# Kernel optimization log

Measured on AMD Instinct MI355X. Metric: run time of the kernel, lower is better.

## Reference

```python
import jax, jax.numpy as jnp
import numpy as np

B, T, D, H = 4, 4096, 2048, 128  # head_size = embedding_size // num_heads = 2048 // 16

def setup_inputs() -> dict:
    key = jax.random.key(0)
    kx, kq, kk, kv = jax.random.split(key, 4)
    x = jax.random.normal(kx, (B, T, D), dtype=jnp.float32)
    # Dense kernels with normal(0.01) init as in the module
    Wq = 0.01 * jax.random.normal(kq, (D, H), dtype=jnp.float32)
    Wk = 0.01 * jax.random.normal(kk, (D, H), dtype=jnp.float32)
    Wv = 0.01 * jax.random.normal(kv, (D, H), dtype=jnp.float32)
    return {"x": x, "Wq": Wq, "Wk": Wk, "Wv": Wv}

def reference(x, Wq, Wk, Wv):
    # Q/K/V projections: Dense(features=head_size, use_bias=False)
    Q = jnp.einsum('BTD,DH->BTH', x, Wq)
    K = jnp.einsum('BTD,DH->BTH', x, Wk)
    V = jnp.einsum('BTD,DH->BTH', x, Wv)
    scale = 1.0 / jnp.sqrt(jnp.asarray(K.shape[-1], dtype=x.dtype))
    scores = jnp.einsum('BTH,BSH->BTS', Q, K) * scale  # (B, T, T)
    weights = jax.nn.softmax(scores, axis=-1)
    # dropout rate 0.0 (deterministic) -> identity
    out = jnp.einsum('BTS,BSH->BTH', weights, V)  # (B, T, H)
    return out
```

## Files before the change

### kernel.cpp

```cpp
#include <hip/hip_runtime.h>
#include <hip/hip_bf16.h>
#include <math.h>

#define B_ 4
#define T_ 4096
#define D_ 2048
#define H_ 128
#define M_ (B_*T_)

typedef __bf16 bf16;
typedef __attribute__((ext_vector_type(8))) __bf16 bf16x8;
typedef __attribute__((ext_vector_type(4))) float f32x4;
typedef __attribute__((ext_vector_type(16))) float f32x16;

#define MFMA16(a,b,c) __builtin_amdgcn_mfma_f32_16x16x32_bf16(a,b,c,0,0,0)
#define MFMA32(a,b,c) __builtin_amdgcn_mfma_f32_32x32x16_bf16(a,b,c,0,0,0)

typedef __attribute__((address_space(3))) unsigned int lds_u32_t;
typedef const __attribute__((address_space(1))) unsigned int glb_u32_t;

__device__ __forceinline__ void cp16(void* lds, const void* g) {
    __builtin_amdgcn_global_load_lds((glb_u32_t*)g, (lds_u32_t*)lds, 16, 0, 0);
}

#define QOFF   0u
#define KOFF   (4u<<20)
#define VTOFF  (8u<<20)
#define WTOFF  (12u<<20)
#define OPOFF  (14u<<20)
#define LPOFF  (OPOFF + 8388608u)

__global__ __launch_bounds__(256) void cvtw_kernel(
    const float* __restrict__ Wq, const float* __restrict__ Wk,
    const float* __restrict__ Wv, bf16* __restrict__ Wtb)
{
    __shared__ __align__(16) bf16 U[128 * 72];
    const int tid = threadIdx.x;
    const int m  = blockIdx.x >> 5;
    const int kt = blockIdx.x & 31;
    const int k0 = kt * 64;
    const float* W = (m == 0) ? Wq : ((m == 1) ? Wk : Wv);
    const float sc = (m == 0) ? 0.08838834764831845f : 1.0f;

    #pragma unroll
    for (int u = 0; u < 8; u++) {
        int id = tid + u * 256;
        int kr = id >> 5, c4 = id & 31;
        float4 v = *(const float4*)(W + (size_t)(k0 + kr) * H_ + c4 * 4);
        U[(c4*4 + 0) * 72 + kr] = (bf16)(v.x * sc);
        U[(c4*4 + 1) * 72 + kr] = (bf16)(v.y * sc);
        U[(c4*4 + 2) * 72 + kr] = (bf16)(v.z * sc);
        U[(c4*4 + 3) * 72 + kr] = (bf16)(v.w * sc);
    }
    __syncthreads();
    #pragma unroll
    for (int u = 0; u < 4; u++) {
        int id = tid + u * 256;
        int n = id >> 3, kc = id & 7;
        bf16x8 v = *(const bf16x8*)((const char*)U + n * 144 + kc * 16);
        *(bf16x8*)((char*)Wtb + (size_t)m * 524288 + (size_t)n * 4096
                   + k0 * 2 + kc * 16) = v;
    }
}

__global__ __launch_bounds__(256, 1) void proj_kernel(
    const float* __restrict__ X, const bf16* __restrict__ Wtb,
    bf16* __restrict__ Qb, bf16* __restrict__ Kb, bf16* __restrict__ Vtb)
{
    __shared__ __align__(16) char smem[114688];

    const int tid = threadIdx.x;
    const int lane = tid & 63;
    const int ng = tid >> 6;
    const int c31 = lane & 31;
    const int kh = lane >> 5;
    const int m0 = blockIdx.x * 64;

    f32x16 acc[2][3];
    #pragma unroll
    for (int mt = 0; mt < 2; mt++)
        #pragma unroll
        for (int t = 0; t < 3; t++)
            #pragma unroll
            for (int r = 0; r < 16; r++) acc[mt][t][r] = 0.f;


    {
        char* w0 = smem + 16384;
        #pragma unroll
        for (int u = 0; u < 12; u++) {
            int s = tid + u * 256;
            int n = s >> 3, ccs = s & 7;
            int kc = ccs ^ (n & 7);
            int mat = n >> 7, ncol = n & 127;
            cp16(w0 + s * 16,
                 (const char*)Wtb + (size_t)mat * 524288 + (size_t)ncol * 4096 + kc * 16);
        }
        #pragma unroll
        for (int u = 0; u < 2; u++) {
            int id = tid + u * 256;
            int r = id >> 3, cc = id & 7;
            const float* src = X + (size_t)(m0 + r) * D_ + cc * 8;
            float4 v0 = *(const float4*)src;
            float4 v1 = *(const float4*)(src + 4);
            union { bf16 h[8]; uint4 u4; } pk;
            pk.h[0]=(bf16)v0.x; pk.h[1]=(bf16)v0.y; pk.h[2]=(bf16)v0.z; pk.h[3]=(bf16)v0.w;
            pk.h[4]=(bf16)v1.x; pk.h[5]=(bf16)v1.y; pk.h[6]=(bf16)v1.z; pk.h[7]=(bf16)v1.w;
            int slot = r * 8 + (cc ^ (r & 7));
            *(uint4*)(smem + slot * 16) = pk.u4;
        }
    }
    __syncthreads();

    for (int it = 0; it < 32; it++) {
        const int cur = it & 1, nxt = cur ^ 1;
        const int k1 = (it + 1) * 64;
        char* xcur = smem + cur * 8192;
        char* xnxt = smem + nxt * 8192;
        char* wcur = smem + 16384 + cur * 49152;
        char* wnxt = smem + 16384 + nxt * 49152;
        float4 xv[4];
        if (it < 31) {
            #pragma unroll
            for (int u = 0; u < 12; u++) {
                int s = tid + u * 256;
                int n = s >> 3, ccs = s & 7;
                int kc = ccs ^ (n & 7);
                int mat = n >> 7, ncol = n & 127;
                cp16(wnxt + s * 16,
                     (const char*)Wtb + (size_t)mat * 524288 + (size_t)ncol * 4096
                     + k1 * 2 + kc * 16);
            }
            #pragma unroll
            for (int u = 0; u < 2; u++) {
                int id = tid + u * 256;
                int r = id >> 3, cc = id & 7;
                const float* src = X + (size_t)(m0 + r) * D_ + k1 + cc * 8;
                xv[u*2+0] = *(const float4*)src;
                xv[u*2+1] = *(const float4*)(src + 4);
            }
        }
        #pragma unroll
        for (int ks = 0; ks < 4; ks++) {
            const int kc = ks * 2 + kh;
            bf16x8 a[2], bq[3];
            #pragma unroll
            for (int mt = 0; mt < 2; mt++) {
                int r = mt * 32 + c31;
                int slot = r * 8 + (kc ^ (r & 7));
                a[mt] = *(const bf16x8*)(xcur + slot * 16);
            }
            #pragma unroll
            for (int t = 0; t < 3; t++) {
                int n = ng * 96 + t * 32 + c31;
                int slot = n * 8 + (kc ^ (n & 7));
                bq[t] = *(const bf16x8*)(wcur + slot * 16);
            }
            #pragma unroll
            for (int mt = 0; mt < 2; mt++)
                #pragma unroll
                for (int t = 0; t < 3; t++)
                    acc[mt][t] = MFMA32(a[mt], bq[t], acc[mt][t]);
        }
        if (it < 31) {
            #pragma unroll
            for (int u = 0; u < 2; u++) {
                int id = tid + u * 256;
                int r = id >> 3, cc = id & 7;
                union { bf16 h[8]; uint4 u4; } pk;
                float4 v0 = xv[u*2+0], v1 = xv[u*2+1];
                pk.h[0]=(bf16)v0.x; pk.h[1]=(bf16)v0.y; pk.h[2]=(bf16)v0.z; pk.h[3]=(bf16)v0.w;
                pk.h[4]=(bf16)v1.x; pk.h[5]=(bf16)v1.y; pk.h[6]=(bf16)v1.z; pk.h[7]=(bf16)v1.w;
                int slot = r * 8 + (cc ^ (r & 7));
                *(uint4*)(xnxt + slot * 16) = pk.u4;
            }
        }
        __syncthreads();
    }

    #pragma unroll
    for (int mt = 0; mt < 2; mt++) {
        #pragma unroll
        for (int t = 0; t < 3; t++) {
            int nb = ng * 96 + t * 32;
            if ((nb >> 7) == 2) {
                int ncol = (nb & 127) + c31;
                #pragma unroll
                for (int g = 0; g < 4; g++) {
                    int m = m0 + mt * 32 + g * 8 + kh * 4;
                    union { bf16 h[4]; uint2 u2; } pk;
                    #pragma unroll
                    for (int e = 0; e < 4; e++)
                        pk.h[e] = (bf16)acc[mt][t][g*4 + e];
                    *(uint2*)((char*)Vtb + (size_t)ncol * 32768 + (size_t)m * 2) = pk.u2;
                }
            }
        }
    }
    bf16* U = (bf16*)smem;
    #pragma unroll
    for (int mat = 0; mat < 2; mat++) {
        __syncthreads();
        #pragma unroll
        for (int mt = 0; mt < 2; mt++) {
            #pragma unroll
            for (int t = 0; t < 3; t++) {
                int nb = ng * 96 + t * 32;
                if ((nb >> 7) == mat) {
                    int lcol = (nb & 127) + c31;
                    #pragma unroll
                    for (int r = 0; r < 16; r++) {
                        int row = (r & 3) + 8 * (r >> 2) + 4 * kh;
                        U[(mt*32 + row) * 136 + lcol] = (bf16)acc[mt][t][r];
                    }
                }
            }
        }
        __syncthreads();
        bf16* og = (mat == 0) ? Qb : Kb;
        #pragma unroll
        for (int u = 0; u < 4; u++) {
            int id = tid + u * 256;
            int rr = id >> 4, cc = id & 15;
            bf16x8 v = *(const bf16x8*)((const char*)U + rr * 272 + cc * 16);
            *(bf16x8*)((char*)og + (size_t)(m0 + rr) * 256 + cc * 16) = v;
        }
    }
}

__global__ __launch_bounds__(256) void attn_kernel(
    const bf16* __restrict__ Qb, const bf16* __restrict__ Kb,
    const bf16* __restrict__ Vtb,
    float* __restrict__ Out0, float* __restrict__ Opart1,
    float* __restrict__ lpart)
{
    __shared__ __align__(16) char Ks[16384];
    __shared__ __align__(16) char Vs[16384];
    __shared__ __align__(16) char Ps[9216];

    const int tid = threadIdx.x;
    const int w = tid >> 6, lane = tid & 63;
    const int c = lane & 15, quad = lane >> 4;

    const int bx = blockIdx.x;
    const int qt = bx & 63;
    const int b  = (bx >> 6) & 3;
    const int ks = bx >> 8;
    const int row0 = b*T_ + qt*64;

    bf16x8 qf[4];
    {
        const char* qrow = (const char*)Qb + (size_t)(row0 + w*16 + c)*256 + quad*16;
        #pragma unroll
        for (int kk = 0; kk < 4; kk++)
            qf[kk] = *(const bf16x8*)(qrow + kk*64);
    }

    f32x4 o[8];
    #pragma unroll
    for (int i = 0; i < 8; i++) o[i] = (f32x4){0.f,0.f,0.f,0.f};
    float lsum[4] = {0.f, 0.f, 0.f, 0.f};

    for (int it = 0; it < 32; it++) {
        const int k0 = ks*2048 + it*64;
        __syncthreads();
        #pragma unroll
        for (int u = 0; u < 4; u++) {
            int s = tid + u*256;
            int r = s >> 4, csw = s & 15;
            int cg = (csw & 8) | ((csw ^ r) & 7);
            const char* src = (const char*)Kb + (size_t)(b*T_ + k0 + r)*256 + cg*16;
            cp16(Ks + s*16, src);
        }
        #pragma unroll
        for (int u = 0; u < 4; u++) {
            int s = tid + u*256;
            int h = s >> 3, ccsw = s & 7;
            int cc = (ccsw ^ h) & 7;
            const char* src = (const char*)Vtb + (size_t)h*32768
                            + (size_t)(b*T_ + k0)*2 + cc*16;
            cp16(Vs + s*16, src);
        }
        __syncthreads();

        #pragma unroll
        for (int ct = 0; ct < 4; ct++) {
            f32x4 s4 = (f32x4){0.f,0.f,0.f,0.f};
            int row = ct*16 + c;
            #pragma unroll
            for (int kk = 0; kk < 4; kk++) {
                int cg = quad + 4*kk;
                int slot = row*16 + (((cg ^ row) & 7) | (cg & 8));
                bf16x8 kf = *(const bf16x8*)(Ks + slot*16);
                s4 = MFMA16(qf[kk], kf, s4);
            }
            #pragma unroll
            for (int r = 0; r < 4; r++) {
                float p = __expf(s4[r]);
                lsum[r] += p;
                ((bf16*)Ps)[(w*16 + quad*4 + r)*72 + ct*16 + c] = (bf16)p;
            }
        }
        #pragma unroll
        for (int kk = 0; kk < 2; kk++) {
            bf16x8 pf = *(const bf16x8*)(Ps + (w*16 + c)*144 + quad*16 + kk*64);
            #pragma unroll
            for (int ct = 0; ct < 8; ct++) {
                int n = ct*16 + c;
                int cc = quad + 4*kk;
                int slot = n*8 + ((cc ^ n) & 7);
                bf16x8 vf = *(const bf16x8*)(Vs + slot*16);
                o[ct] = MFMA16(pf, vf, o[ct]);
            }
        }
    }

    #pragma unroll
    for (int r = 0; r < 4; r++) {
        float v = lsum[r];
        #pragma unroll
        for (int off = 1; off < 16; off <<= 1)
            v += __shfl_xor(v, off, 64);
        if (c == 0)
            lpart[ks*M_ + row0 + w*16 + quad*4 + r] = v;
    }
    float* Od = (ks == 0) ? Out0 : Opart1;
    #pragma unroll
    for (int ct = 0; ct < 8; ct++)
        #pragma unroll
        for (int r = 0; r < 4; r++)
            Od[(size_t)(row0 + w*16 + quad*4 + r)*H_ + ct*16 + c] = o[ct][r];
}

__global__ __launch_bounds__(256) void merge_kernel(
    float* __restrict__ Out, const float* __restrict__ Op1,
    const float* __restrict__ lp)
{
    int id = blockIdx.x * 256 + threadIdx.x;
    int row = id >> 5;
    float inv = 1.0f / (lp[row] + lp[M_ + row]);
    float4 a = *(const float4*)(Out + (size_t)id*4);
    float4 bq = *(const float4*)(Op1 + (size_t)id*4);
    float4 rr;
    rr.x = (a.x + bq.x) * inv; rr.y = (a.y + bq.y) * inv;
    rr.z = (a.z + bq.z) * inv; rr.w = (a.w + bq.w) * inv;
    *(float4*)(Out + (size_t)id*4) = rr;
}

extern "C" void kernel_launch(void* const* d_in, const int* in_sizes, int n_in,
                              void* d_out, int out_size, void* d_ws, size_t ws_size,
                              hipStream_t stream) {
    const float* x  = (const float*)d_in[0];
    const float* Wq = (const float*)d_in[1];
    const float* Wk = (const float*)d_in[2];
    const float* Wv = (const float*)d_in[3];
    float* outp = (float*)d_out;
    char* ws = (char*)d_ws;

    bf16* Qb  = (bf16*)(ws + QOFF);
    bf16* Kb  = (bf16*)(ws + KOFF);
    bf16* Vtb = (bf16*)(ws + VTOFF);
    bf16* Wtb = (bf16*)(ws + WTOFF);
    float* Op1 = (float*)(ws + OPOFF);
    float* lp  = (float*)(ws + LPOFF);

    cvtw_kernel<<<96, 256, 0, stream>>>(Wq, Wk, Wv, Wtb);
    proj_kernel<<<M_/64, 256, 0, stream>>>(x, Wtb, Qb, Kb, Vtb);
    attn_kernel<<<512, 256, 0, stream>>>(Qb, Kb, Vtb, outp, Op1, lp);
    merge_kernel<<<2048, 256, 0, stream>>>(outp, Op1, lp);
}
```

Before: 291.3 us.

## Restructure projection to 512 threads and attention to 32x32 MFMA with double buffering

The projection kernel moves to 512 threads, with each wave owning one 32-row half and three 32-column tiles, which halves per-thread accumulators and loads. The attention kernel switches from 16x16 to 32x32 MFMA tiles, double-buffers the K/V tiles in LDS so the next tile loads while the current one is computed, and splits the key and output-column work across wave pairs. Row sums are reduced through LDS. Both changes aim to raise MFMA efficiency and hide global-load latency, at the cost of more LDS (two blocks per CU of 114KB may not fit for proj) and an extra barrier per iteration.

```diff
diff --git a/kernel.cpp b/kernel.cpp
--- a/kernel.cpp
+++ b/kernel.cpp
@@ -13,7 +13,6 @@
 typedef __attribute__((ext_vector_type(4))) float f32x4;
 typedef __attribute__((ext_vector_type(16))) float f32x16;
 
-#define MFMA16(a,b,c) __builtin_amdgcn_mfma_f32_16x16x32_bf16(a,b,c,0,0,0)
 #define MFMA32(a,b,c) __builtin_amdgcn_mfma_f32_32x32x16_bf16(a,b,c,0,0,0)
 
 typedef __attribute__((address_space(3))) unsigned int lds_u32_t;
@@ -63,67 +62,57 @@
     }
 }
 
-__global__ __launch_bounds__(256, 1) void proj_kernel(
+__global__ __launch_bounds__(512, 2) void proj_kernel(
     const float* __restrict__ X, const bf16* __restrict__ Wtb,
     bf16* __restrict__ Qb, bf16* __restrict__ Kb, bf16* __restrict__ Vtb)
 {
     __shared__ __align__(16) char smem[114688];
 
     const int tid = threadIdx.x;
-    const int lane = tid & 63;
-    const int ng = tid >> 6;
-    const int c31 = lane & 31;
-    const int kh = lane >> 5;
+    const int w = tid >> 6, lane = tid & 63;
+    const int c31 = lane & 31, kh = lane >> 5;
+    const int mh = w >> 2;
+    const int ng = w & 3;
     const int m0 = blockIdx.x * 64;
 
-    f32x16 acc[2][3];
-    #pragma unroll
-    for (int mt = 0; mt < 2; mt++)
-        #pragma unroll
-        for (int t = 0; t < 3; t++)
-            #pragma unroll
-            for (int r = 0; r < 16; r++) acc[mt][t][r] = 0.f;
-
-
+    f32x16 acc[3];
+    #pragma unroll
+    for (int t = 0; t < 3; t++)
+        #pragma unroll
+        for (int r = 0; r < 16; r++) acc[t][r] = 0.f;
+
+    #pragma unroll
+    for (int u = 0; u < 6; u++) {
+        int s = tid + u * 512;
+        int n = s >> 3, ccs = s & 7;
+        int kc = ccs ^ (n & 7);
+        int mat = n >> 7, ncol = n & 127;
+        cp16(smem + 16384 + s * 16,
+             (const char*)Wtb + (size_t)mat * 524288 + (size_t)ncol * 4096 + kc * 16);
+    }
     {
-        char* w0 = smem + 16384;
-        #pragma unroll
-        for (int u = 0; u < 12; u++) {
-            int s = tid + u * 256;
-            int n = s >> 3, ccs = s & 7;
-            int kc = ccs ^ (n & 7);
-            int mat = n >> 7, ncol = n & 127;
-            cp16(w0 + s * 16,
-                 (const char*)Wtb + (size_t)mat * 524288 + (size_t)ncol * 4096 + kc * 16);
-        }
-        #pragma unroll
-        for (int u = 0; u < 2; u++) {
-            int id = tid + u * 256;
-            int r = id >> 3, cc = id & 7;
-            const float* src = X + (size_t)(m0 + r) * D_ + cc * 8;
-            float4 v0 = *(const float4*)src;
-            float4 v1 = *(const float4*)(src + 4);
-            union { bf16 h[8]; uint4 u4; } pk;
-            pk.h[0]=(bf16)v0.x; pk.h[1]=(bf16)v0.y; pk.h[2]=(bf16)v0.z; pk.h[3]=(bf16)v0.w;
-            pk.h[4]=(bf16)v1.x; pk.h[5]=(bf16)v1.y; pk.h[6]=(bf16)v1.z; pk.h[7]=(bf16)v1.w;
-            int slot = r * 8 + (cc ^ (r & 7));
-            *(uint4*)(smem + slot * 16) = pk.u4;
-        }
+        int r = tid >> 3, cc = tid & 7;
+        const float* src = X + (size_t)(m0 + r) * D_ + cc * 8;
+        float4 v0 = *(const float4*)src;
+        float4 v1 = *(const float4*)(src + 4);
+        union { bf16 h[8]; uint4 u4; } pk;
+        pk.h[0]=(bf16)v0.x; pk.h[1]=(bf16)v0.y; pk.h[2]=(bf16)v0.z; pk.h[3]=(bf16)v0.w;
+        pk.h[4]=(bf16)v1.x; pk.h[5]=(bf16)v1.y; pk.h[6]=(bf16)v1.z; pk.h[7]=(bf16)v1.w;
+        *(uint4*)(smem + (r * 8 + (cc ^ (r & 7))) * 16) = pk.u4;
     }
     __syncthreads();
 
     for (int it = 0; it < 32; it++) {
-        const int cur = it & 1, nxt = cur ^ 1;
-        const int k1 = (it + 1) * 64;
+        const int cur = it & 1;
         char* xcur = smem + cur * 8192;
-        char* xnxt = smem + nxt * 8192;
         char* wcur = smem + 16384 + cur * 49152;
-        char* wnxt = smem + 16384 + nxt * 49152;
-        float4 xv[4];
+        float4 xv0, xv1;
         if (it < 31) {
-            #pragma unroll
-            for (int u = 0; u < 12; u++) {
-                int s = tid + u * 256;
+            const int k1 = (it + 1) * 64;
+            char* wnxt = smem + 16384 + (cur ^ 1) * 49152;
+            #pragma unroll
+            for (int u = 0; u < 6; u++) {
+                int s = tid + u * 512;
                 int n = s >> 3, ccs = s & 7;
                 int kc = ccs ^ (n & 7);
                 int mat = n >> 7, ncol = n & 127;
@@ -131,96 +120,70 @@
                      (const char*)Wtb + (size_t)mat * 524288 + (size_t)ncol * 4096
                      + k1 * 2 + kc * 16);
             }
-            #pragma unroll
-            for (int u = 0; u < 2; u++) {
-                int id = tid + u * 256;
-                int r = id >> 3, cc = id & 7;
-                const float* src = X + (size_t)(m0 + r) * D_ + k1 + cc * 8;
-                xv[u*2+0] = *(const float4*)src;
-                xv[u*2+1] = *(const float4*)(src + 4);
-            }
-        }
-        #pragma unroll
-        for (int ks = 0; ks < 4; ks++) {
-            const int kc = ks * 2 + kh;
-            bf16x8 a[2], bq[3];
-            #pragma unroll
-            for (int mt = 0; mt < 2; mt++) {
-                int r = mt * 32 + c31;
-                int slot = r * 8 + (kc ^ (r & 7));
-                a[mt] = *(const bf16x8*)(xcur + slot * 16);
-            }
+            int r = tid >> 3, cc = tid & 7;
+            const float* src = X + (size_t)(m0 + r) * D_ + k1 + cc * 8;
+            xv0 = *(const float4*)src;
+            xv1 = *(const float4*)(src + 4);
+        }
+        #pragma unroll
+        for (int s = 0; s < 4; s++) {
+            int c = s * 2 + kh;
+            int rr = mh * 32 + c31;
+            bf16x8 af = *(const bf16x8*)(xcur + (rr * 8 + (c ^ (rr & 7))) * 16);
             #pragma unroll
             for (int t = 0; t < 3; t++) {
                 int n = ng * 96 + t * 32 + c31;
-                int slot = n * 8 + (kc ^ (n & 7));
-                bq[t] = *(const bf16x8*)(wcur + slot * 16);
-            }
-            #pragma unroll
-            for (int mt = 0; mt < 2; mt++)
+                bf16x8 bfr = *(const bf16x8*)(wcur + (n * 8 + (c ^ (n & 7))) * 16);
+                acc[t] = MFMA32(af, bfr, acc[t]);
+            }
+        }
+        if (it < 31) {
+            char* xnxt = smem + (cur ^ 1) * 8192;
+            int r = tid >> 3, cc = tid & 7;
+            union { bf16 h[8]; uint4 u4; } pk;
+            pk.h[0]=(bf16)xv0.x; pk.h[1]=(bf16)xv0.y; pk.h[2]=(bf16)xv0.z; pk.h[3]=(bf16)xv0.w;
+            pk.h[4]=(bf16)xv1.x; pk.h[5]=(bf16)xv1.y; pk.h[6]=(bf16)xv1.z; pk.h[7]=(bf16)xv1.w;
+            *(uint4*)(xnxt + (r * 8 + (cc ^ (r & 7))) * 16) = pk.u4;
+        }
+        __syncthreads();
+    }
+
+    #pragma unroll
+    for (int t = 0; t < 3; t++) {
+        int nb = ng * 96 + t * 32;
+        if ((nb >> 7) == 2) {
+            int ncol = (nb & 127) + c31;
+            #pragma unroll
+            for (int g = 0; g < 4; g++) {
+                int m = m0 + mh * 32 + g * 8 + kh * 4;
+                union { bf16 h[4]; uint2 u2; } pk;
                 #pragma unroll
-                for (int t = 0; t < 3; t++)
-                    acc[mt][t] = MFMA32(a[mt], bq[t], acc[mt][t]);
-        }
-        if (it < 31) {
-            #pragma unroll
-            for (int u = 0; u < 2; u++) {
-                int id = tid + u * 256;
-                int r = id >> 3, cc = id & 7;
-                union { bf16 h[8]; uint4 u4; } pk;
-                float4 v0 = xv[u*2+0], v1 = xv[u*2+1];
-                pk.h[0]=(bf16)v0.x; pk.h[1]=(bf16)v0.y; pk.h[2]=(bf16)v0.z; pk.h[3]=(bf16)v0.w;
-                pk.h[4]=(bf16)v1.x; pk.h[5]=(bf16)v1.y; pk.h[6]=(bf16)v1.z; pk.h[7]=(bf16)v1.w;
-                int slot = r * 8 + (cc ^ (r & 7));
-                *(uint4*)(xnxt + slot * 16) = pk.u4;
-            }
-        }
-        __syncthreads();
-    }
-
-    #pragma unroll
-    for (int mt = 0; mt < 2; mt++) {
+                for (int e = 0; e < 4; e++) pk.h[e] = (bf16)acc[t][g*4 + e];
+                *(uint2*)((char*)Vtb + (size_t)ncol * 32768 + (size_t)m * 2) = pk.u2;
+            }
+        }
+    }
+    bf16* U = (bf16*)smem;
+    #pragma unroll
+    for (int mat = 0; mat < 2; mat++) {
+        __syncthreads();
         #pragma unroll
         for (int t = 0; t < 3; t++) {
             int nb = ng * 96 + t * 32;
-            if ((nb >> 7) == 2) {
-                int ncol = (nb & 127) + c31;
+            if ((nb >> 7) == mat) {
+                int lcol = (nb & 127) + c31;
                 #pragma unroll
-                for (int g = 0; g < 4; g++) {
-                    int m = m0 + mt * 32 + g * 8 + kh * 4;
-                    union { bf16 h[4]; uint2 u2; } pk;
-                    #pragma unroll
-                    for (int e = 0; e < 4; e++)
-                        pk.h[e] = (bf16)acc[mt][t][g*4 + e];
-                    *(uint2*)((char*)Vtb + (size_t)ncol * 32768 + (size_t)m * 2) = pk.u2;
+                for (int r = 0; r < 16; r++) {
+                    int row = mh * 32 + (r & 3) + 8 * (r >> 2) + 4 * kh;
+                    U[row * 136 + lcol] = (bf16)acc[t][r];
                 }
             }
         }
-    }
-    bf16* U = (bf16*)smem;
-    #pragma unroll
-    for (int mat = 0; mat < 2; mat++) {
-        __syncthreads();
-        #pragma unroll
-        for (int mt = 0; mt < 2; mt++) {
-            #pragma unroll
-            for (int t = 0; t < 3; t++) {
-                int nb = ng * 96 + t * 32;
-                if ((nb >> 7) == mat) {
-                    int lcol = (nb & 127) + c31;
-                    #pragma unroll
-                    for (int r = 0; r < 16; r++) {
-                        int row = (r & 3) + 8 * (r >> 2) + 4 * kh;
-                        U[(mt*32 + row) * 136 + lcol] = (bf16)acc[mt][t][r];
-                    }
-                }
-            }
-        }
         __syncthreads();
         bf16* og = (mat == 0) ? Qb : Kb;
         #pragma unroll
-        for (int u = 0; u < 4; u++) {
-            int id = tid + u * 256;
+        for (int u = 0; u < 2; u++) {
+            int id = tid + u * 512;
             int rr = id >> 4, cc = id & 15;
             bf16x8 v = *(const bf16x8*)((const char*)U + rr * 272 + cc * 16);
             *(bf16x8*)((char*)og + (size_t)(m0 + rr) * 256 + cc * 16) = v;
@@ -228,108 +191,144 @@
     }
 }
 
-__global__ __launch_bounds__(256) void attn_kernel(
+__global__ __launch_bounds__(256, 2) void attn_kernel(
     const bf16* __restrict__ Qb, const bf16* __restrict__ Kb,
     const bf16* __restrict__ Vtb,
     float* __restrict__ Out0, float* __restrict__ Opart1,
     float* __restrict__ lpart)
 {
-    __shared__ __align__(16) char Ks[16384];
-    __shared__ __align__(16) char Vs[16384];
-    __shared__ __align__(16) char Ps[9216];
+    __shared__ __align__(16) char smem[75264];
 
     const int tid = threadIdx.x;
     const int w = tid >> 6, lane = tid & 63;
-    const int c = lane & 15, quad = lane >> 4;
+    const int c31 = lane & 31, kh = lane >> 5;
 
     const int bx = blockIdx.x;
     const int qt = bx & 63;
     const int b  = (bx >> 6) & 3;
     const int ks = bx >> 8;
     const int row0 = b*T_ + qt*64;
-
-    bf16x8 qf[4];
+    const int kvrow = b*T_ + ks*2048;
+
+    const int mh  = w >> 1;
+    const int kh2 = w & 1;
+    const int nq0 = (w & 1) * 2;
+
+    bf16x8 qf[8];
     {
-        const char* qrow = (const char*)Qb + (size_t)(row0 + w*16 + c)*256 + quad*16;
-        #pragma unroll
-        for (int kk = 0; kk < 4; kk++)
-            qf[kk] = *(const bf16x8*)(qrow + kk*64);
-    }
-
-    f32x4 o[8];
-    #pragma unroll
-    for (int i = 0; i < 8; i++) o[i] = (f32x4){0.f,0.f,0.f,0.f};
-    float lsum[4] = {0.f, 0.f, 0.f, 0.f};
+        const char* qrow = (const char*)Qb + (size_t)(row0 + mh*32 + c31)*256 + kh*16;
+        #pragma unroll
+        for (int s = 0; s < 8; s++)
+            qf[s] = *(const bf16x8*)(qrow + s*32);
+    }
+
+    f32x16 o0, o1;
+    #pragma unroll
+    for (int r = 0; r < 16; r++) { o0[r] = 0.f; o1[r] = 0.f; }
+    float lsum[16];
+    #pragma unroll
+    for (int r = 0; r < 16; r++) lsum[r] = 0.f;
+
+    #pragma unroll
+    for (int u = 0; u < 4; u++) {
+        int s = tid + u*256;
+        int r = s >> 4, csw = s & 15;
+        int cg = (csw & 8) | ((csw ^ r) & 7);
+        cp16(smem + s*16, (const char*)Kb + (size_t)(kvrow + r)*256 + cg*16);
+    }
+    #pragma unroll
+    for (int u = 0; u < 4; u++) {
+        int s = tid + u*256;
+        int h = s >> 3, ccsw = s & 7;
+        int cc = (ccsw ^ h) & 7;
+        cp16(smem + 32768 + s*16,
+             (const char*)Vtb + (size_t)h*32768 + (size_t)kvrow*2 + cc*16);
+    }
+    __syncthreads();
 
     for (int it = 0; it < 32; it++) {
-        const int k0 = ks*2048 + it*64;
-        __syncthreads();
-        #pragma unroll
-        for (int u = 0; u < 4; u++) {
-            int s = tid + u*256;
-            int r = s >> 4, csw = s & 15;
-            int cg = (csw & 8) | ((csw ^ r) & 7);
-            const char* src = (const char*)Kb + (size_t)(b*T_ + k0 + r)*256 + cg*16;
-            cp16(Ks + s*16, src);
-        }
-        #pragma unroll
-        for (int u = 0; u < 4; u++) {
-            int s = tid + u*256;
-            int h = s >> 3, ccsw = s & 7;
-            int cc = (ccsw ^ h) & 7;
-            const char* src = (const char*)Vtb + (size_t)h*32768
-                            + (size_t)(b*T_ + k0)*2 + cc*16;
-            cp16(Vs + s*16, src);
-        }
-        __syncthreads();
-
-        #pragma unroll
-        for (int ct = 0; ct < 4; ct++) {
-            f32x4 s4 = (f32x4){0.f,0.f,0.f,0.f};
-            int row = ct*16 + c;
-            #pragma unroll
-            for (int kk = 0; kk < 4; kk++) {
-                int cg = quad + 4*kk;
-                int slot = row*16 + (((cg ^ row) & 7) | (cg & 8));
-                bf16x8 kf = *(const bf16x8*)(Ks + slot*16);
-                s4 = MFMA16(qf[kk], kf, s4);
-            }
-            #pragma unroll
-            for (int r = 0; r < 4; r++) {
-                float p = __expf(s4[r]);
-                lsum[r] += p;
-                ((bf16*)Ps)[(w*16 + quad*4 + r)*72 + ct*16 + c] = (bf16)p;
-            }
-        }
-        #pragma unroll
-        for (int kk = 0; kk < 2; kk++) {
-            bf16x8 pf = *(const bf16x8*)(Ps + (w*16 + c)*144 + quad*16 + kk*64);
-            #pragma unroll
-            for (int ct = 0; ct < 8; ct++) {
-                int n = ct*16 + c;
-                int cc = quad + 4*kk;
-                int slot = n*8 + ((cc ^ n) & 7);
-                bf16x8 vf = *(const bf16x8*)(Vs + slot*16);
-                o[ct] = MFMA16(pf, vf, o[ct]);
-            }
-        }
-    }
-
-    #pragma unroll
-    for (int r = 0; r < 4; r++) {
+        const int cur = it & 1;
+        char* ksb = smem + cur*16384;
+        char* vsb = smem + 32768 + cur*16384;
+        if (it < 31) {
+            const int knx = kvrow + (it + 1)*64;
+            char* kn = smem + (cur ^ 1)*16384;
+            char* vn = smem + 32768 + (cur ^ 1)*16384;
+            #pragma unroll
+            for (int u = 0; u < 4; u++) {
+                int s = tid + u*256;
+                int r = s >> 4, csw = s & 15;
+                int cg = (csw & 8) | ((csw ^ r) & 7);
+                cp16(kn + s*16, (const char*)Kb + (size_t)(knx + r)*256 + cg*16);
+            }
+            #pragma unroll
+            for (int u = 0; u < 4; u++) {
+                int s = tid + u*256;
+                int h = s >> 3, ccsw = s & 7;
+                int cc = (ccsw ^ h) & 7;
+                cp16(vn + s*16,
+                     (const char*)Vtb + (size_t)h*32768 + (size_t)knx*2 + cc*16);
+            }
+        }
+
+        f32x16 sacc;
+        #pragma unroll
+        for (int r = 0; r < 16; r++) sacc[r] = 0.f;
+        const int key = kh2*32 + c31;
+        #pragma unroll
+        for (int s = 0; s < 8; s++) {
+            int ck = s*2 + kh;
+            int slot = key*16 + ((ck & 8) | ((ck ^ key) & 7));
+            bf16x8 kf = *(const bf16x8*)(ksb + slot*16);
+            sacc = MFMA32(qf[s], kf, sacc);
+        }
+        bf16* Pp = (bf16*)(smem + 65536);
+        #pragma unroll
+        for (int r = 0; r < 16; r++) {
+            float p = __expf(sacc[r]);
+            lsum[r] += p;
+            int irow = (r & 3) + 8*(r >> 2) + 4*kh;
+            Pp[(mh*32 + irow)*72 + key] = (bf16)p;
+        }
+        __syncthreads();
+
+        #pragma unroll
+        for (int s2 = 0; s2 < 4; s2++) {
+            bf16x8 pf = *(const bf16x8*)(smem + 65536
+                           + (mh*32 + c31)*144 + s2*32 + kh*16);
+            int cv = s2*2 + kh;
+            int n0 = nq0*32 + c31;
+            int n1 = n0 + 32;
+            bf16x8 vf0 = *(const bf16x8*)(vsb + (n0*8 + ((cv ^ n0) & 7))*16);
+            bf16x8 vf1 = *(const bf16x8*)(vsb + (n1*8 + ((cv ^ n1) & 7))*16);
+            o0 = MFMA32(pf, vf0, o0);
+            o1 = MFMA32(pf, vf1, o1);
+        }
+        __syncthreads();
+    }
+
+    #pragma unroll
+    for (int r = 0; r < 16; r++) {
         float v = lsum[r];
-        #pragma unroll
-        for (int off = 1; off < 16; off <<= 1)
-            v += __shfl_xor(v, off, 64);
-        if (c == 0)
-            lpart[ks*M_ + row0 + w*16 + quad*4 + r] = v;
+        v += __shfl_xor(v, 1); v += __shfl_xor(v, 2); v += __shfl_xor(v, 4);
+        v += __shfl_xor(v, 8); v += __shfl_xor(v, 16);
+        if (c31 == 0) {
+            int irow = (r & 3) + 8*(r >> 2) + 4*kh;
+            ((float*)(smem + 74752))[kh2*64 + mh*32 + irow] = v;
+        }
+    }
+    __syncthreads();
+    if (tid < 64) {
+        const float* lr = (const float*)(smem + 74752);
+        lpart[ks*M_ + row0 + tid] = lr[tid] + lr[64 + tid];
     }
     float* Od = (ks == 0) ? Out0 : Opart1;
     #pragma unroll
-    for (int ct = 0; ct < 8; ct++)
-        #pragma unroll
-        for (int r = 0; r < 4; r++)
-            Od[(size_t)(row0 + w*16 + quad*4 + r)*H_ + ct*16 + c] = o[ct][r];
+    for (int r = 0; r < 16; r++) {
+        int m = mh*32 + (r & 3) + 8*(r >> 2) + 4*kh;
+        Od[(size_t)(row0 + m)*H_ + nq0*32 + c31] = o0[r];
+        Od[(size_t)(row0 + m)*H_ + nq0*32 + 32 + c31] = o1[r];
+    }
 }
 
 __global__ __launch_bounds__(256) void merge_kernel(
@@ -365,7 +364,7 @@
     float* lp  = (float*)(ws + LPOFF);
 
     cvtw_kernel<<<96, 256, 0, stream>>>(Wq, Wk, Wv, Wtb);
-    proj_kernel<<<M_/64, 256, 0, stream>>>(x, Wtb, Qb, Kb, Vtb);
+    proj_kernel<<<M_/64, 512, 0, stream>>>(x, Wtb, Qb, Kb, Vtb);
     attn_kernel<<<512, 256, 0, stream>>>(Qb, Kb, Vtb, outp, Op1, lp);
     merge_kernel<<<2048, 256, 0, stream>>>(outp, Op1, lp);
 }
```

New measurement: 273.4 us. 1.07x faster.
